# Performance work log

Hardware: AMD Instinct MI355X
Metric: run time of the kernel (lower is better)

## Reference

```python
import jax, jax.numpy as jnp
import numpy as np
from jax import lax

# Module constants (from init_kwargs)
B, C = 2, 64            # batch, in_channel
H, W, D = 64, 64, 64    # size
GROUPS = 2


def setup_inputs() -> dict:
    key = jax.random.key(0)
    ks = jax.random.split(key, 4)
    x = jax.random.normal(ks[0], (B, H * W * D, C), dtype=jnp.float32)
    # TransverseConv: Conv3d(2, W*2, (H,3,3), pad (0,1,1)) -> weight (O,I,kD,kH,kW)
    w_t = jax.random.normal(ks[1], (W * GROUPS, GROUPS, H, 3, 3), dtype=jnp.float32) * 0.02
    b_t = jnp.zeros((W * GROUPS,), jnp.float32)
    # CoronalConv: Conv3d(2, W*2, (3,3,D), pad (1,1,0))
    w_c = jax.random.normal(ks[2], (W * GROUPS, GROUPS, 3, 3, D), dtype=jnp.float32) * 0.02
    b_c = jnp.zeros((W * GROUPS,), jnp.float32)
    # map: Conv3d(2C, C, 1) stored as dense (C, 2C)
    w_map = jax.random.normal(ks[3], (C, 2 * C), dtype=jnp.float32) * 0.02
    b_map = jnp.zeros((C,), jnp.float32)
    return {"x": x, "w_t": w_t, "b_t": b_t, "w_c": w_c, "b_c": b_c,
            "w_map": w_map, "b_map": b_map}


def _forward(x, w_t, b_t, w_c, b_c, w_map, b_map):
    Bx, N, Cx = x.shape
    xg = x.transpose(0, 2, 1).reshape(Bx, Cx, H, W, D)   # (B,C,H,W,D)
    shortcut = xg
    xr = xg.reshape(Bx * Cx // GROUPS, GROUPS, H, W, D)
    dn = ('NCDHW', 'OIDHW', 'NCDHW')
    # Transverse: kernel spans full H -> output (B*C/2, 2W, 1, W, D)
    tans = lax.conv_general_dilated(xr, w_t, (1, 1, 1), [(0, 0), (1, 1), (1, 1)],
                                    dimension_numbers=dn)
    tans = tans + b_t[None, :, None, None, None]
    tans = tans.reshape(Bx, Cx, W, W, D)                 # (B,C,W,W,D)
    # Coronal: kernel spans full D -> output (B*C/2, 2W, H, W, 1)
    cor = lax.conv_general_dilated(xr, w_c, (1, 1, 1), [(1, 1), (1, 1), (0, 0)],
                                   dimension_numbers=dn)
    cor = cor + b_c[None, :, None, None, None]
    cor = cor.reshape(Bx, Cx, W, H, W)                   # (B,C,W,H,W)
    t1 = tans.transpose(0, 1, 3, 2, 4)                   # (B,C,W,W,D)
    c1 = cor.transpose(0, 1, 4, 3, 2)                    # (B,C,W,H,W)
    f = jnp.matmul(c1, t1).transpose(0, 1, 3, 2, 4)      # (B,C,H,W,D)
    attn = jnp.matmul(cor, tans).transpose(0, 1, 3, 2, 4)  # (B,C,H,W,D)
    cat = jnp.concatenate([shortcut * f, attn], axis=1)  # (B,2C,H,W,D)
    mapped = jnp.einsum('bkhwd,ck->bchwd', cat, w_map) + b_map[None, :, None, None, None]
    out = jax.nn.gelu(mapped, approximate=False)         # torch nn.GELU = exact erf
    return out.reshape(Bx, Cx, -1).transpose(0, 2, 1)    # (B,N,C)


def reference(x, w_t, b_t, w_c, b_c, w_map, b_map):
    return _forward(x, w_t, b_t, w_c, b_c, w_map, b_map)
```

## Files before the change

kernel.cpp:

```cpp
#include <hip/hip_runtime.h>
#include <hip/hip_bf16.h>
#include <math.h>

#define HWD 262144

typedef __attribute__((ext_vector_type(8))) short bf16x8;
typedef __attribute__((ext_vector_type(16))) float f32x16;

__global__ void k_prep(const float* __restrict__ w_t, const float* __restrict__ w_c,
                       const float* __restrict__ w_map,
                       __hip_bfloat16* __restrict__ A_t, __hip_bfloat16* __restrict__ A_c,
                       __hip_bfloat16* __restrict__ Wb) {
    int i = blockIdx.x * 256 + threadIdx.x;
    if (i < 147456) {
        int kk = i & 15, oc = (i >> 4) & 127, ks = i >> 11;
        int z4 = ks & 3, kq = ks >> 2;
        int g = kq / 9, tap = kq - 9 * g;
        int z = z4 * 16 + kk;
        A_t[i] = __float2bfloat16(w_t[((oc * 2 + g) * 64 + z) * 9 + tap]);
        A_c[i] = __float2bfloat16(w_c[((oc * 2 + g) * 9 + tap) * 64 + z]);
    }
    if (i < 8192) {
        Wb[i] = __float2bfloat16(w_map[i]);
    }
}

__device__ inline void pack_row_bf16(__hip_bfloat16* dst, const float* src) {
    unsigned short u[16];
#pragma unroll
    for (int j = 0; j < 16; ++j) {
        __hip_bfloat16 h = __float2bfloat16(src[j]);
        u[j] = *reinterpret_cast<unsigned short*>(&h);
    }
    uint4* q = reinterpret_cast<uint4*>(dst);
    q[0] = *reinterpret_cast<const uint4*>(&u[0]);
    q[1] = *reinterpret_cast<const uint4*>(&u[8]);
}

__global__ void k_trans_c(const float* __restrict__ x, __hip_bfloat16* __restrict__ Xc) {
    __shared__ float tile[64][65];
    int b = blockIdx.y;
    long n0 = (long)blockIdx.x * 64;
    int t = threadIdx.x;
    const float4* xp4 = (const float4*)(x + ((long)b * HWD + n0) * 64);
#pragma unroll
    for (int j = 0; j < 4; ++j) {
        int f4i = j * 256 + t;
        float4 v = xp4[f4i];
        int row = f4i >> 4;
        int c4 = (f4i & 15) * 4;
        tile[c4 + 0][row] = v.x;
        tile[c4 + 1][row] = v.y;
        tile[c4 + 2][row] = v.z;
        tile[c4 + 3][row] = v.w;
    }
    __syncthreads();
    int c = t >> 2, sub = t & 3;
    pack_row_bf16(Xc + (long)(b * 64 + c) * HWD + n0 + sub * 16, &tile[c][sub * 16]);
}

__global__ void k_trans_t(const float* __restrict__ x, __hip_bfloat16* __restrict__ Xt) {
    __shared__ float tile[64][65];
    int b = blockIdx.y;
    int wd = blockIdx.x;
    int t = threadIdx.x;
#pragma unroll
    for (int j = 0; j < 4; ++j) {
        int f4i = j * 256 + t;
        int h = f4i >> 4;
        int c4 = (f4i & 15) * 4;
        float4 v = *(const float4*)(x + ((long)b * HWD + (long)h * 4096 + wd) * 64 + c4);
        tile[c4 + 0][h] = v.x;
        tile[c4 + 1][h] = v.y;
        tile[c4 + 2][h] = v.z;
        tile[c4 + 3][h] = v.w;
    }
    __syncthreads();
    int c = t >> 2, sub = t & 3;
    pack_row_bf16(Xt + (long)(b * 64 + c) * HWD + (long)wd * 64 + sub * 16, &tile[c][sub * 16]);
}

__global__ __launch_bounds__(256, 4) void k_conv_mfma(
        const __hip_bfloat16* __restrict__ X, const __hip_bfloat16* __restrict__ Aglob,
        const float* __restrict__ bias, float* __restrict__ Out) {
    int L = blockIdx.x;
    int grp = (L & 7) * 8 + ((L >> 3) >> 5);
    int pt = (L >> 3) & 31;
    int b = grp >> 5, ch = grp & 31;
    int p0 = pt * 2;
    const __hip_bfloat16* Xg = X + ((long)(b * 64 + 2 * ch)) * HWD;
    int t = threadIdx.x;
    int lane = t & 63, wv = t >> 6;

    __shared__ short Asm[128 * 24];
    __shared__ short Bsm[128 * 24];

    f32x16 acc00 = {0}, acc01 = {0}, acc10 = {0}, acc11 = {0};

    int srow = t >> 1, shalf = t & 1;
    int pr = srow >> 6, q = srow & 63;
    int O0 = (wv >> 1) * 64;
    int N0 = (wv & 1) * 64;
    int lrow = lane & 31, lq = lane >> 5;

    for (int ks = 0; ks < 72; ++ks) {
        int z4 = ks & 3, kq = ks >> 2;
        int g = kq / 9, tap = kq - 9 * g;
        int r = tap / 3, s = tap - 3 * r;
        uint4 av = *(const uint4*)(Aglob + ks * 2048 + t * 8);
        int pp = p0 + pr + r - 1, qq = q + s - 1;
        uint4 bv = {0u, 0u, 0u, 0u};
        if (pp >= 0 && pp < 64 && qq >= 0 && qq < 64)
            bv = *(const uint4*)(Xg + (long)g * HWD + ((pp << 6) + qq) * 64 + z4 * 16 + shalf * 8);
        __syncthreads();
        *(uint4*)(Asm + srow * 24 + shalf * 8) = av;
        *(uint4*)(Bsm + srow * 24 + shalf * 8) = bv;
        __syncthreads();
        bf16x8 a0 = *(const bf16x8*)(Asm + (O0 + lrow) * 24 + lq * 8);
        bf16x8 a1 = *(const bf16x8*)(Asm + (O0 + 32 + lrow) * 24 + lq * 8);
        bf16x8 b0 = *(const bf16x8*)(Bsm + (N0 + lrow) * 24 + lq * 8);
        bf16x8 b1 = *(const bf16x8*)(Bsm + (N0 + 32 + lrow) * 24 + lq * 8);
        acc00 = __builtin_amdgcn_mfma_f32_32x32x16_bf16(a0, b0, acc00, 0, 0, 0);
        acc01 = __builtin_amdgcn_mfma_f32_32x32x16_bf16(a0, b1, acc01, 0, 0, 0);
        acc10 = __builtin_amdgcn_mfma_f32_32x32x16_bf16(a1, b0, acc10, 0, 0, 0);
        acc11 = __builtin_amdgcn_mfma_f32_32x32x16_bf16(a1, b1, acc11, 0, 0, 0);
    }

    long base0 = ((long)(b * 64 + 2 * ch)) * HWD + (long)p0 * 64;
    int n0l = N0 + lrow, n1l = N0 + 32 + lrow;
    long noff0 = (long)(n0l >> 6) * 64 + (n0l & 63);
    long noff1 = (long)(n1l >> 6) * 64 + (n1l & 63);
#pragma unroll
    for (int reg = 0; reg < 16; ++reg) {
        int row = (reg & 3) + 8 * (reg >> 2) + 4 * lq;
        int oc0 = O0 + row, oc1 = O0 + 32 + row;
        long cb0 = base0 + (long)(oc0 >> 6) * HWD + (long)(oc0 & 63) * 4096;
        long cb1 = base0 + (long)(oc1 >> 6) * HWD + (long)(oc1 & 63) * 4096;
        float bs0 = bias[oc0], bs1 = bias[oc1];
        Out[cb0 + noff0] = acc00[reg] + bs0;
        Out[cb0 + noff1] = acc01[reg] + bs0;
        Out[cb1 + noff0] = acc10[reg] + bs1;
        Out[cb1 + noff1] = acc11[reg] + bs1;
    }
}

__global__ void k_attn(const float* __restrict__ Cc, const float* __restrict__ T,
                       __hip_bfloat16* __restrict__ At) {
    __shared__ float As[64][65];
    __shared__ float Bs[64][64];
    int bc = blockIdx.x >> 6, w2 = blockIdx.x & 63;
    const float* Ap = Cc + ((long)bc * 64 + w2) * 4096;
    const float* Bp = T + ((long)bc * 64 + w2) * 4096;
    int t = threadIdx.x;
#pragma unroll
    for (int e0 = 0; e0 < 4096; e0 += 256) {
        int e = e0 + t;
        int r = e >> 6, q = e & 63;
        As[r][q] = Ap[e];
        Bs[r][q] = Bp[e];
    }
    __syncthreads();
    int h = t >> 2, dg = (t & 3) * 16;
    f32x16 acc = {0};
    for (int k = 0; k < 64; ++k) {
        float a = As[h][k];
#pragma unroll
        for (int i = 0; i < 16; ++i)
            acc[i] = fmaf(a, Bs[k][dg + i], acc[i]);
    }
    float tmp[16];
#pragma unroll
    for (int i = 0; i < 16; ++i) tmp[i] = acc[i];
    pack_row_bf16(At + (long)bc * HWD + (long)h * 4096 + w2 * 64 + dg, tmp);
}

__global__ __launch_bounds__(512, 4) void k_f(const float* __restrict__ Cc,
        const float* __restrict__ T, __hip_bfloat16* __restrict__ F) {
    __shared__ float As[16][64][8];
    __shared__ float Bs[16][8][68];
    int L = blockIdx.x;
    int xcd = L & 7, j = L >> 3;
    int bc = xcd * 16 + (j >> 3), wt = j & 7;
    const float* Ab = Cc + (long)bc * HWD + wt * 8;
    const float* Bb = T + (long)bc * HWD + wt * 8 * 64;
    int t = threadIdx.x;
    int w = t & 7, h = t >> 3;
    f32x16 acc0 = {0}, acc1 = {0}, acc2 = {0}, acc3 = {0};

    for (int w2c = 0; w2c < 4; ++w2c) {
        __syncthreads();
#pragma unroll
        for (int i = 0; i < 4; ++i) {
            int f = i * 512 + t;
            int half = f & 1, hh = (f >> 1) & 63, kk = f >> 7;
            float4 v = *(const float4*)(Ab + (long)(w2c * 16 + kk) * 4096 + hh * 64 + half * 4);
            *(float4*)&As[kk][hh][half * 4] = v;
        }
#pragma unroll
        for (int i = 0; i < 4; ++i) {
            int f = i * 512 + t;
            int d4 = f & 15, ww = (f >> 4) & 7, kk = f >> 7;
            float4 v = *(const float4*)(Bb + (long)(w2c * 16 + kk) * 4096 + ww * 64 + d4 * 4);
            *(float4*)&Bs[kk][ww][d4 * 4] = v;
        }
        __syncthreads();
        for (int kk = 0; kk < 16; ++kk) {
            float a = As[kk][h][w];
            const float* br = &Bs[kk][w][0];
#pragma unroll
            for (int i = 0; i < 16; ++i) {
                acc0[i] = fmaf(a, br[i], acc0[i]);
                acc1[i] = fmaf(a, br[16 + i], acc1[i]);
                acc2[i] = fmaf(a, br[32 + i], acc2[i]);
                acc3[i] = fmaf(a, br[48 + i], acc3[i]);
            }
        }
    }
    __hip_bfloat16* Fp = F + (long)bc * HWD + (long)h * 4096 + (wt * 8 + w) * 64;
    float tmp[16];
#pragma unroll
    for (int i = 0; i < 16; ++i) tmp[i] = acc0[i];
    pack_row_bf16(Fp, tmp);
#pragma unroll
    for (int i = 0; i < 16; ++i) tmp[i] = acc1[i];
    pack_row_bf16(Fp + 16, tmp);
#pragma unroll
    for (int i = 0; i < 16; ++i) tmp[i] = acc2[i];
    pack_row_bf16(Fp + 32, tmp);
#pragma unroll
    for (int i = 0; i < 16; ++i) tmp[i] = acc3[i];
    pack_row_bf16(Fp + 48, tmp);
}

__global__ __launch_bounds__(256, 4) void k_map(const float* __restrict__ x,
        const __hip_bfloat16* __restrict__ F, const __hip_bfloat16* __restrict__ At,
        const __hip_bfloat16* __restrict__ Wb, const float* __restrict__ b_map,
        float* __restrict__ out) {
    __shared__ float xs[16][257];
    __shared__ __hip_bfloat16 fa[16][264];
    __shared__ short Pl[256][24];
    __shared__ short Wt[64][136];

    int t = threadIdx.x;
    long n0 = (long)blockIdx.x * 256;
    int b = (int)(n0 >> 18);
    long nn0 = n0 & (HWD - 1);
    const float* xblk = x + n0 * 64;
    const __hip_bfloat16* Fb = F + (long)b * 64 * HWD + nn0;
    const __hip_bfloat16* Ab = At + (long)b * 64 * HWD + nn0;

#pragma unroll
    for (int i = 0; i < 4; ++i) {
        int e = i * 256 + t;
        int c = e >> 4, kk = (e & 15) * 8;
        *(uint4*)&Wt[c][kk] = *(const uint4*)((const short*)Wb + c * 128 + kk);
    }

    int lane = t & 63, wv = t >> 6;
    int lrow = lane & 31, lhalf = lane >> 5;
    f32x16 acc00 = {0}, acc01 = {0}, acc10 = {0}, acc11 = {0};

    for (int kc = 0; kc < 8; ++kc) {
        __syncthreads();
        if (kc < 4) {
#pragma unroll
            for (int i2 = 0; i2 < 4; ++i2) {
                int f = i2 * 256 + t;
                int nr = f >> 2, j4 = (f & 3) * 4;
                float4 v = *(const float4*)(xblk + nr * 64 + kc * 16 + j4);
                xs[j4 + 0][nr] = v.x;
                xs[j4 + 1][nr] = v.y;
                xs[j4 + 2][nr] = v.z;
                xs[j4 + 3][nr] = v.w;
            }
#pragma unroll
            for (int it = 0; it < 2; ++it) {
                int idx = it * 256 + t;
                int row = idx >> 5, seg = idx & 31;
                *(uint4*)&fa[row][seg * 8] =
                    *(const uint4*)(Fb + (long)(kc * 16 + row) * HWD + seg * 8);
            }
        } else {
#pragma unroll
            for (int it = 0; it < 2; ++it) {
                int idx = it * 256 + t;
                int row = idx >> 5, seg = idx & 31;
                *(uint4*)&fa[row][seg * 8] =
                    *(const uint4*)(Ab + (long)((kc - 4) * 16 + row) * HWD + seg * 8);
            }
        }
        __syncthreads();
        unsigned short pv[16];
        if (kc < 4) {
#pragma unroll
            for (int k2 = 0; k2 < 16; ++k2) {
                float p = xs[k2][t] * __bfloat162float(fa[k2][t]);
                __hip_bfloat16 h = __float2bfloat16(p);
                pv[k2] = *reinterpret_cast<unsigned short*>(&h);
            }
        } else {
#pragma unroll
            for (int k2 = 0; k2 < 16; ++k2)
                pv[k2] = *reinterpret_cast<const unsigned short*>(&fa[k2][t]);
        }
        *(uint4*)&Pl[t][0] = *(uint4*)&pv[0];
        *(uint4*)&Pl[t][8] = *(uint4*)&pv[8];
        __syncthreads();
        bf16x8 a0 = *(const bf16x8*)&Pl[wv * 64 + lrow][lhalf * 8];
        bf16x8 a1 = *(const bf16x8*)&Pl[wv * 64 + 32 + lrow][lhalf * 8];
        bf16x8 b0 = *(const bf16x8*)&Wt[lrow][kc * 16 + lhalf * 8];
        bf16x8 b1 = *(const bf16x8*)&Wt[32 + lrow][kc * 16 + lhalf * 8];
        acc00 = __builtin_amdgcn_mfma_f32_32x32x16_bf16(a0, b0, acc00, 0, 0, 0);
        acc01 = __builtin_amdgcn_mfma_f32_32x32x16_bf16(a0, b1, acc01, 0, 0, 0);
        acc10 = __builtin_amdgcn_mfma_f32_32x32x16_bf16(a1, b0, acc10, 0, 0, 0);
        acc11 = __builtin_amdgcn_mfma_f32_32x32x16_bf16(a1, b1, acc11, 0, 0, 0);
    }

    float bs0 = b_map[lrow];
    float bs1 = b_map[32 + lrow];
    const float inv_sqrt2 = 0.70710678118654752440f;
    float* ob = out + (n0 + wv * 64) * 64;
#pragma unroll
    for (int reg = 0; reg < 16; ++reg) {
        int nrow = (reg & 3) + 8 * (reg >> 2) + 4 * lhalf;
        float v00 = acc00[reg] + bs0;
        float v01 = acc01[reg] + bs1;
        float v10 = acc10[reg] + bs0;
        float v11 = acc11[reg] + bs1;
        v00 = 0.5f * v00 * (1.f + erff(v00 * inv_sqrt2));
        v01 = 0.5f * v01 * (1.f + erff(v01 * inv_sqrt2));
        v10 = 0.5f * v10 * (1.f + erff(v10 * inv_sqrt2));
        v11 = 0.5f * v11 * (1.f + erff(v11 * inv_sqrt2));
        ob[(long)nrow * 64 + lrow] = v00;
        ob[(long)nrow * 64 + 32 + lrow] = v01;
        ob[(long)(32 + nrow) * 64 + lrow] = v10;
        ob[(long)(32 + nrow) * 64 + 32 + lrow] = v11;
    }
}

extern "C" void kernel_launch(void* const* d_in, const int* in_sizes, int n_in,
                              void* d_out, int out_size, void* d_ws, size_t ws_size,
                              hipStream_t stream) {
    const float* x     = (const float*)d_in[0];
    const float* w_t   = (const float*)d_in[1];
    const float* b_t   = (const float*)d_in[2];
    const float* w_c   = (const float*)d_in[3];
    const float* b_c   = (const float*)d_in[4];
    const float* w_map = (const float*)d_in[5];
    const float* b_map = (const float*)d_in[6];
    float* out = (float*)d_out;
    float* ws = (float*)d_ws;

    __hip_bfloat16* Xc = (__hip_bfloat16*)ws;
    __hip_bfloat16* Xt = (__hip_bfloat16*)(ws + 16777216L);
    float* T = ws + 33554432L;
    float* Cc = out;
    __hip_bfloat16* A_t = (__hip_bfloat16*)(ws + 67108864L);
    __hip_bfloat16* A_c = (__hip_bfloat16*)(ws + 67182592L);
    __hip_bfloat16* Wb = (__hip_bfloat16*)(ws + 67256320L);
    __hip_bfloat16* At_bf = Xc;
    __hip_bfloat16* F_bf = Xt;

    hipLaunchKernelGGL(k_prep, dim3(576), dim3(256), 0, stream, w_t, w_c, w_map, A_t, A_c, Wb);
    hipLaunchKernelGGL(k_trans_c, dim3(4096, 2), dim3(256), 0, stream, x, Xc);
    hipLaunchKernelGGL(k_trans_t, dim3(4096, 2), dim3(256), 0, stream, x, Xt);
    hipLaunchKernelGGL(k_conv_mfma, dim3(2048), dim3(256), 0, stream, Xt, A_t, b_t, T);
    hipLaunchKernelGGL(k_conv_mfma, dim3(2048), dim3(256), 0, stream, Xc, A_c, b_c, Cc);
    hipLaunchKernelGGL(k_attn, dim3(8192), dim3(256), 0, stream, Cc, T, At_bf);
    hipLaunchKernelGGL(k_f, dim3(1024), dim3(512), 0, stream, Cc, T, F_bf);
    hipLaunchKernelGGL(k_map, dim3(2048), dim3(256), 0, stream, x, F_bf, At_bf, Wb, b_map, out);
}
```

Baseline: 799.6 us.

## Double-buffer conv B tiles, read A from global, split bf16 layout by z4

The bf16 transposed input layout now splits the 64-wide z axis into four 16-element slabs stored as separate planes, so each conv k-step reads a contiguous slab. The conv kernel drops the shared-memory staging of the weight tile, reading A fragments straight from global/L2, and double-buffers the B tile so the next step's global load overlaps the current MFMAs with one barrier per step instead of two. This trades more global traffic for weights and extra LDS for fewer syncs. Other consumers of Xc/Xt in the unseen code must agree with the new layout.

```diff
diff --git a/kernel.cpp b/kernel.cpp
--- a/kernel.cpp
+++ b/kernel.cpp
@@ -56,7 +56,8 @@
     }
     __syncthreads();
     int c = t >> 2, sub = t & 3;
-    pack_row_bf16(Xc + (long)(b * 64 + c) * HWD + n0 + sub * 16, &tile[c][sub * 16]);
+    pack_row_bf16(Xc + (long)(b * 64 + c) * HWD + sub * 65536 + (long)blockIdx.x * 16,
+                  &tile[c][sub * 16]);
 }
 
 __global__ void k_trans_t(const float* __restrict__ x, __hip_bfloat16* __restrict__ Xt) {
@@ -77,7 +78,8 @@
     }
     __syncthreads();
     int c = t >> 2, sub = t & 3;
-    pack_row_bf16(Xt + (long)(b * 64 + c) * HWD + (long)wd * 64 + sub * 16, &tile[c][sub * 16]);
+    pack_row_bf16(Xt + (long)(b * 64 + c) * HWD + sub * 65536 + (long)wd * 16,
+                  &tile[c][sub * 16]);
 }
 
 __global__ __launch_bounds__(256, 4) void k_conv_mfma(
@@ -92,8 +94,7 @@
     int t = threadIdx.x;
     int lane = t & 63, wv = t >> 6;
 
-    __shared__ short Asm[128 * 24];
-    __shared__ short Bsm[128 * 24];
+    __shared__ __align__(16) short Bsm[2 * 128 * 24];
 
     f32x16 acc00 = {0}, acc01 = {0}, acc10 = {0}, acc11 = {0};
 
@@ -102,28 +103,43 @@
     int O0 = (wv >> 1) * 64;
     int N0 = (wv & 1) * 64;
     int lrow = lane & 31, lq = lane >> 5;
-
-    for (int ks = 0; ks < 72; ++ks) {
+    const short* Ag = (const short*)Aglob;
+
+    auto loadB = [&](int ks) -> uint4 {
         int z4 = ks & 3, kq = ks >> 2;
         int g = kq / 9, tap = kq - 9 * g;
         int r = tap / 3, s = tap - 3 * r;
-        uint4 av = *(const uint4*)(Aglob + ks * 2048 + t * 8);
         int pp = p0 + pr + r - 1, qq = q + s - 1;
         uint4 bv = {0u, 0u, 0u, 0u};
         if (pp >= 0 && pp < 64 && qq >= 0 && qq < 64)
-            bv = *(const uint4*)(Xg + (long)g * HWD + ((pp << 6) + qq) * 64 + z4 * 16 + shalf * 8);
-        __syncthreads();
-        *(uint4*)(Asm + srow * 24 + shalf * 8) = av;
-        *(uint4*)(Bsm + srow * 24 + shalf * 8) = bv;
-        __syncthreads();
-        bf16x8 a0 = *(const bf16x8*)(Asm + (O0 + lrow) * 24 + lq * 8);
-        bf16x8 a1 = *(const bf16x8*)(Asm + (O0 + 32 + lrow) * 24 + lq * 8);
-        bf16x8 b0 = *(const bf16x8*)(Bsm + (N0 + lrow) * 24 + lq * 8);
-        bf16x8 b1 = *(const bf16x8*)(Bsm + (N0 + 32 + lrow) * 24 + lq * 8);
+            bv = *(const uint4*)(Xg + (long)g * HWD + z4 * 65536 + ((pp << 6) + qq) * 16 + shalf * 8);
+        return bv;
+    };
+
+    {
+        uint4 b0v = loadB(0);
+        *(uint4*)(Bsm + srow * 24 + shalf * 8) = b0v;
+    }
+    __syncthreads();
+
+    int buf = 0;
+    for (int ks = 0; ks < 72; ++ks) {
+        uint4 bnext;
+        if (ks < 71) bnext = loadB(ks + 1);
+        const short* Bc = Bsm + buf * 3072;
+        bf16x8 a0 = *(const bf16x8*)(Ag + ks * 2048 + (O0 + lrow) * 16 + lq * 8);
+        bf16x8 a1 = *(const bf16x8*)(Ag + ks * 2048 + (O0 + 32 + lrow) * 16 + lq * 8);
+        bf16x8 b0 = *(const bf16x8*)(Bc + (N0 + lrow) * 24 + lq * 8);
+        bf16x8 b1 = *(const bf16x8*)(Bc + (N0 + 32 + lrow) * 24 + lq * 8);
         acc00 = __builtin_amdgcn_mfma_f32_32x32x16_bf16(a0, b0, acc00, 0, 0, 0);
         acc01 = __builtin_amdgcn_mfma_f32_32x32x16_bf16(a0, b1, acc01, 0, 0, 0);
         acc10 = __builtin_amdgcn_mfma_f32_32x32x16_bf16(a1, b0, acc10, 0, 0, 0);
         acc11 = __builtin_amdgcn_mfma_f32_32x32x16_bf16(a1, b1, acc11, 0, 0, 0);
+        if (ks < 71) {
+            *(uint4*)(Bsm + (buf ^ 1) * 3072 + srow * 24 + shalf * 8) = bnext;
+            __syncthreads();
+            buf ^= 1;
+        }
     }
 
     long base0 = ((long)(b * 64 + 2 * ch)) * HWD + (long)p0 * 64;
```

Result: slower. 872.3 us (+9.1%).

## Re-layout bf16 inputs as z-blocked planes and load MFMA operands directly from global

Applied to the files above, without the earlier changes.

The transpose kernels now write the bf16 copies of x in a blocked layout: four z-slabs of 16 elements, each slab contiguous over (h,w). The conv kernel can then read each MFMA operand fragment straight from global memory into registers, dropping the shared-memory staging and both per-step __syncthreads. The transposes also do 4x more work per block and convert to bf16 before the LDS transpose. The catch is that the conv loop relies on cache hits and compiler latency hiding, with no explicit shared reuse of the weight and activation tiles across waves.

```diff
diff --git a/kernel.cpp b/kernel.cpp
--- a/kernel.cpp
+++ b/kernel.cpp
@@ -6,6 +6,11 @@
 
 typedef __attribute__((ext_vector_type(8))) short bf16x8;
 typedef __attribute__((ext_vector_type(16))) float f32x16;
+
+__device__ inline unsigned short bfu(float f) {
+    __hip_bfloat16 h = __float2bfloat16(f);
+    return *reinterpret_cast<unsigned short*>(&h);
+}
 
 __global__ void k_prep(const float* __restrict__ w_t, const float* __restrict__ w_c,
                        const float* __restrict__ w_map,
@@ -28,56 +33,70 @@
 __device__ inline void pack_row_bf16(__hip_bfloat16* dst, const float* src) {
     unsigned short u[16];
 #pragma unroll
-    for (int j = 0; j < 16; ++j) {
-        __hip_bfloat16 h = __float2bfloat16(src[j]);
-        u[j] = *reinterpret_cast<unsigned short*>(&h);
-    }
+    for (int j = 0; j < 16; ++j) u[j] = bfu(src[j]);
     uint4* q = reinterpret_cast<uint4*>(dst);
     q[0] = *reinterpret_cast<const uint4*>(&u[0]);
     q[1] = *reinterpret_cast<const uint4*>(&u[8]);
 }
 
 __global__ void k_trans_c(const float* __restrict__ x, __hip_bfloat16* __restrict__ Xc) {
-    __shared__ float tile[64][65];
+    __shared__ unsigned short tile[256][68];
     int b = blockIdx.y;
-    long n0 = (long)blockIdx.x * 64;
+    long n0 = (long)blockIdx.x * 256;
     int t = threadIdx.x;
     const float4* xp4 = (const float4*)(x + ((long)b * HWD + n0) * 64);
 #pragma unroll
-    for (int j = 0; j < 4; ++j) {
-        int f4i = j * 256 + t;
+    for (int i = 0; i < 16; ++i) {
+        int f4i = i * 256 + t;
         float4 v = xp4[f4i];
-        int row = f4i >> 4;
-        int c4 = (f4i & 15) * 4;
-        tile[c4 + 0][row] = v.x;
-        tile[c4 + 1][row] = v.y;
-        tile[c4 + 2][row] = v.z;
-        tile[c4 + 3][row] = v.w;
+        int nl = f4i >> 4, c4 = (f4i & 15) * 4;
+        ushort4 u;
+        u.x = bfu(v.x); u.y = bfu(v.y); u.z = bfu(v.z); u.w = bfu(v.w);
+        *(ushort4*)&tile[nl][c4] = u;
     }
     __syncthreads();
-    int c = t >> 2, sub = t & 3;
-    pack_row_bf16(Xc + (long)(b * 64 + c) * HWD + n0 + sub * 16, &tile[c][sub * 16]);
+    int c = t >> 2, hwl = t & 3;
+    int hw0 = blockIdx.x * 4;
+    __hip_bfloat16* dst0 = Xc + (long)(b * 64 + c) * HWD + (long)(hw0 + hwl) * 16;
+#pragma unroll
+    for (int z4 = 0; z4 < 4; ++z4) {
+        unsigned short u[16];
+#pragma unroll
+        for (int j = 0; j < 16; ++j) u[j] = tile[hwl * 64 + z4 * 16 + j][c];
+        __hip_bfloat16* dst = dst0 + z4 * 65536;
+        *(uint4*)dst = *(const uint4*)&u[0];
+        *(uint4*)(dst + 8) = *(const uint4*)&u[8];
+    }
 }
 
 __global__ void k_trans_t(const float* __restrict__ x, __hip_bfloat16* __restrict__ Xt) {
-    __shared__ float tile[64][65];
+    __shared__ unsigned short tile[256][68];
     int b = blockIdx.y;
-    int wd = blockIdx.x;
-    int t = threadIdx.x;
-#pragma unroll
-    for (int j = 0; j < 4; ++j) {
-        int f4i = j * 256 + t;
-        int h = f4i >> 4;
-        int c4 = (f4i & 15) * 4;
-        float4 v = *(const float4*)(x + ((long)b * HWD + (long)h * 4096 + wd) * 64 + c4);
-        tile[c4 + 0][h] = v.x;
-        tile[c4 + 1][h] = v.y;
-        tile[c4 + 2][h] = v.z;
-        tile[c4 + 3][h] = v.w;
+    int wd0 = blockIdx.x * 4;
+    int t = threadIdx.x;
+    const float* xb = x + (long)b * HWD * 64 + (long)wd0 * 64;
+#pragma unroll
+    for (int i = 0; i < 16; ++i) {
+        int idx = i * 256 + t;
+        int h = idx >> 6, f = idx & 63;
+        float4 v = *(const float4*)(xb + (long)h * 262144 + f * 4);
+        int wdl = f >> 4, c4 = (f & 15) * 4;
+        ushort4 u;
+        u.x = bfu(v.x); u.y = bfu(v.y); u.z = bfu(v.z); u.w = bfu(v.w);
+        *(ushort4*)&tile[wdl * 64 + h][c4] = u;
     }
     __syncthreads();
-    int c = t >> 2, sub = t & 3;
-    pack_row_bf16(Xt + (long)(b * 64 + c) * HWD + (long)wd * 64 + sub * 16, &tile[c][sub * 16]);
+    int c = t >> 2, wdl = t & 3;
+    __hip_bfloat16* dst0 = Xt + (long)(b * 64 + c) * HWD + (long)(wd0 + wdl) * 16;
+#pragma unroll
+    for (int z4 = 0; z4 < 4; ++z4) {
+        unsigned short u[16];
+#pragma unroll
+        for (int j = 0; j < 16; ++j) u[j] = tile[wdl * 64 + z4 * 16 + j][c];
+        __hip_bfloat16* dst = dst0 + z4 * 65536;
+        *(uint4*)dst = *(const uint4*)&u[0];
+        *(uint4*)(dst + 8) = *(const uint4*)&u[8];
+    }
 }
 
 __global__ __launch_bounds__(256, 4) void k_conv_mfma(
@@ -88,42 +107,51 @@
     int pt = (L >> 3) & 31;
     int b = grp >> 5, ch = grp & 31;
     int p0 = pt * 2;
-    const __hip_bfloat16* Xg = X + ((long)(b * 64 + 2 * ch)) * HWD;
+    const short* Xg = (const short*)(X + ((long)(b * 64 + 2 * ch)) * HWD);
+    const short* Ag = (const short*)Aglob;
     int t = threadIdx.x;
     int lane = t & 63, wv = t >> 6;
-
-    __shared__ short Asm[128 * 24];
-    __shared__ short Bsm[128 * 24];
-
-    f32x16 acc00 = {0}, acc01 = {0}, acc10 = {0}, acc11 = {0};
-
-    int srow = t >> 1, shalf = t & 1;
-    int pr = srow >> 6, q = srow & 63;
     int O0 = (wv >> 1) * 64;
     int N0 = (wv & 1) * 64;
     int lrow = lane & 31, lq = lane >> 5;
-
-    for (int ks = 0; ks < 72; ++ks) {
-        int z4 = ks & 3, kq = ks >> 2;
-        int g = kq / 9, tap = kq - 9 * g;
+    int pr = N0 >> 6;
+
+    f32x16 acc00 = {0}, acc01 = {0}, acc10 = {0}, acc11 = {0};
+
+    const short* Ap = Ag + (O0 + lrow) * 16 + lq * 8;
+    const uint4 zero4 = {0u, 0u, 0u, 0u};
+
+    for (int kq = 0; kq < 18; ++kq) {
+        int g = (kq >= 9) ? 1 : 0;
+        int tap = kq - 9 * g;
         int r = tap / 3, s = tap - 3 * r;
-        uint4 av = *(const uint4*)(Aglob + ks * 2048 + t * 8);
-        int pp = p0 + pr + r - 1, qq = q + s - 1;
-        uint4 bv = {0u, 0u, 0u, 0u};
-        if (pp >= 0 && pp < 64 && qq >= 0 && qq < 64)
-            bv = *(const uint4*)(Xg + (long)g * HWD + ((pp << 6) + qq) * 64 + z4 * 16 + shalf * 8);
-        __syncthreads();
-        *(uint4*)(Asm + srow * 24 + shalf * 8) = av;
-        *(uint4*)(Bsm + srow * 24 + shalf * 8) = bv;
-        __syncthreads();
-        bf16x8 a0 = *(const bf16x8*)(Asm + (O0 + lrow) * 24 + lq * 8);
-        bf16x8 a1 = *(const bf16x8*)(Asm + (O0 + 32 + lrow) * 24 + lq * 8);
-        bf16x8 b0 = *(const bf16x8*)(Bsm + (N0 + lrow) * 24 + lq * 8);
-        bf16x8 b1 = *(const bf16x8*)(Bsm + (N0 + 32 + lrow) * 24 + lq * 8);
-        acc00 = __builtin_amdgcn_mfma_f32_32x32x16_bf16(a0, b0, acc00, 0, 0, 0);
-        acc01 = __builtin_amdgcn_mfma_f32_32x32x16_bf16(a0, b1, acc01, 0, 0, 0);
-        acc10 = __builtin_amdgcn_mfma_f32_32x32x16_bf16(a1, b0, acc10, 0, 0, 0);
-        acc11 = __builtin_amdgcn_mfma_f32_32x32x16_bf16(a1, b1, acc11, 0, 0, 0);
+        int pp = p0 + pr + r - 1;
+        bool pok = (unsigned)pp < 64u;
+        int qq0 = lrow + s - 1;
+        int qq1 = qq0 + 32;
+        bool q0ok = (unsigned)qq0 < 64u;
+        bool q1ok = (unsigned)qq1 < 64u;
+        const short* xb = Xg + (long)g * HWD + pp * 1024 + lq * 8;
+#pragma unroll
+        for (int z4 = 0; z4 < 4; ++z4) {
+            int ks = kq * 4 + z4;
+            uint4 b0u = zero4, b1u = zero4;
+            if (pok) {
+                const short* xz = xb + z4 * 65536;
+                if (q0ok) b0u = *(const uint4*)(xz + qq0 * 16);
+                if (q1ok) b1u = *(const uint4*)(xz + qq1 * 16);
+            }
+            uint4 a0u = *(const uint4*)(Ap + ks * 2048);
+            uint4 a1u = *(const uint4*)(Ap + ks * 2048 + 512);
+            bf16x8 a0 = *(bf16x8*)&a0u;
+            bf16x8 a1 = *(bf16x8*)&a1u;
+            bf16x8 b0 = *(bf16x8*)&b0u;
+            bf16x8 b1 = *(bf16x8*)&b1u;
+            acc00 = __builtin_amdgcn_mfma_f32_32x32x16_bf16(a0, b0, acc00, 0, 0, 0);
+            acc01 = __builtin_amdgcn_mfma_f32_32x32x16_bf16(a0, b1, acc01, 0, 0, 0);
+            acc10 = __builtin_amdgcn_mfma_f32_32x32x16_bf16(a1, b0, acc10, 0, 0, 0);
+            acc11 = __builtin_amdgcn_mfma_f32_32x32x16_bf16(a1, b1, acc11, 0, 0, 0);
+        }
     }
 
     long base0 = ((long)(b * 64 + 2 * ch)) * HWD + (long)p0 * 64;
@@ -295,8 +323,7 @@
 #pragma unroll
             for (int k2 = 0; k2 < 16; ++k2) {
                 float p = xs[k2][t] * __bfloat162float(fa[k2][t]);
-                __hip_bfloat16 h = __float2bfloat16(p);
-                pv[k2] = *reinterpret_cast<unsigned short*>(&h);
+                pv[k2] = bfu(p);
             }
         } else {
 #pragma unroll
@@ -362,8 +389,8 @@
     __hip_bfloat16* F_bf = Xt;
 
     hipLaunchKernelGGL(k_prep, dim3(576), dim3(256), 0, stream, w_t, w_c, w_map, A_t, A_c, Wb);
-    hipLaunchKernelGGL(k_trans_c, dim3(4096, 2), dim3(256), 0, stream, x, Xc);
-    hipLaunchKernelGGL(k_trans_t, dim3(4096, 2), dim3(256), 0, stream, x, Xt);
+    hipLaunchKernelGGL(k_trans_c, dim3(1024, 2), dim3(256), 0, stream, x, Xc);
+    hipLaunchKernelGGL(k_trans_t, dim3(1024, 2), dim3(256), 0, stream, x, Xt);
     hipLaunchKernelGGL(k_conv_mfma, dim3(2048), dim3(256), 0, stream, Xt, A_t, b_t, T);
     hipLaunchKernelGGL(k_conv_mfma, dim3(2048), dim3(256), 0, stream, Xc, A_c, b_c, Cc);
     hipLaunchKernelGGL(k_attn, dim3(8192), dim3(256), 0, stream, Cc, T, At_bf);
```

New measurement: 822.1 us. +2.8%, slower.
